# Kernel optimization log

Hardware: AMD Instinct MI355X
Metric: run time of the kernel (lower is better)

The kernel has to match this reference:

```python
import jax, jax.numpy as jnp
import numpy as np

N, L, A = 64, 196, 512      # batch, image regions, image feature dim
H, E, V = 512, 512, 30000   # lstm hidden, token embedding, vocab
T = 20                      # infer_seq_length
START = 1                   # _start token id


def setup_inputs() -> dict:
    key = jax.random.key(0)
    ks = jax.random.split(key, 16)
    s = lambda i, shape, scale=0.02: (jax.random.normal(ks[i], shape, jnp.float32) * scale)
    return {
        "batch_image_embbeding": jax.random.normal(ks[0], (N, L, A), jnp.float32),
        "emb_table": s(1, (V, E), 0.05),
        "Wh0": s(2, (A, H)), "bh0": jnp.zeros((H,), jnp.float32),
        "Wc0": s(3, (A, H)), "bc0": jnp.zeros((H,), jnp.float32),
        "Wa": s(4, (A, H)), "Ua": s(5, (H, H)), "ba": jnp.zeros((H,), jnp.float32),
        "va": s(6, (H,)),
        "Wb": s(7, (H, 1)), "bb": jnp.zeros((1,), jnp.float32),
        "Wx": s(8, (A + E, 4 * H)), "Wh": s(9, (H, 4 * H)),
        "b_lstm": jnp.zeros((4 * H,), jnp.float32),
        "Wout": s(10, (H, V)), "bout": jnp.zeros((V,), jnp.float32),
    }


def _decode(hl, emb_table, Wh0, bh0, Wc0, bc0, Wa, Ua, ba, va, Wb, bb,
            Wx, Wh, b_lstm, Wout, bout):
    mean_a = jnp.mean(hl, axis=1)                      # [N, A]
    h = jnp.tanh(mean_a @ Wh0 + bh0)                   # fc_init_h
    c = jnp.tanh(mean_a @ Wc0 + bc0)                   # fc_init_c
    tok = jnp.full((hl.shape[0],), START, jnp.int32)
    hl_Wa = jnp.einsum('nla,ah->nlh', hl, Wa)          # precompute attention keys

    def step(carry, _):
        h, c, tok = carry
        x_emb = emb_table[tok]                         # [N, E] embedding lookup
        # additive (Bahdanau) one-step attention
        e = jnp.einsum('nlh,h->nl', jnp.tanh(hl_Wa + (h @ Ua + ba)[:, None, :]), va)
        alpha = jax.nn.softmax(e, axis=-1)             # [N, L]
        z = jnp.einsum('nl,nla->na', alpha, hl)        # [N, A]
        z = z * jax.nn.sigmoid(h @ Wb + bb)            # beta gate
        x = jnp.concatenate([z, x_emb], axis=-1)       # [N, A+E]
        # single-step keras LSTM (gate order i, f, c, o)
        gates = x @ Wx + h @ Wh + b_lstm
        i, f, g, o = jnp.split(gates, 4, axis=-1)
        c = jax.nn.sigmoid(f) * c + jax.nn.sigmoid(i) * jnp.tanh(g)
        h = jax.nn.sigmoid(o) * jnp.tanh(c)
        logits = h @ Wout + bout                       # dropout is identity at inference
        tok = jnp.argmax(logits, axis=-1).astype(jnp.int32)
        return (h, c, tok), tok

    _, toks = jax.lax.scan(step, (h, c, tok), None, length=T)
    return jnp.transpose(toks, (1, 0))                 # [N, T]


def reference(batch_image_embbeding, emb_table, Wh0, bh0, Wc0, bc0, Wa, Ua, ba,
              va, Wb, bb, Wx, Wh, b_lstm, Wout, bout):
    return _decode(batch_image_embbeding, emb_table, Wh0, bh0, Wc0, bc0, Wa, Ua,
                   ba, va, Wb, bb, Wx, Wh, b_lstm, Wout, bout)
```

## Files before the change

kernel.cpp:

```cpp
#include <hip/hip_runtime.h>
#include <math.h>

#define NB   64
#define LL   196
#define AD   512
#define HD   512
#define VD   30000
#define TS   20
#define G4   2048
#define NBL  235
#define NC2  (NBL * 2)

typedef __bf16 bf16x8 __attribute__((ext_vector_type(8)));
typedef float  f32x4  __attribute__((ext_vector_type(4)));

__device__ __forceinline__ float fast_tanh(float x) {
    float e = __builtin_exp2f(x * 2.8853900817779268f);
    return 1.0f - 2.0f / (e + 1.0f);
}
__device__ __forceinline__ float fast_sigmoid(float x) {
    return 1.0f / (1.0f + __builtin_exp2f(-x * 1.4426950408889634f));
}
__device__ __forceinline__ float fast_exp(float x) {
    return __builtin_exp2f(x * 1.4426950408889634f);
}
__device__ __forceinline__ unsigned short f2bf(float f) {
    unsigned int u = __float_as_uint(f);
    u += 0x7fffu + ((u >> 16) & 1u);
    return (unsigned short)(u >> 16);
}
__device__ __forceinline__ void gload_lds16(const void* g, void* l) {
    __builtin_amdgcn_global_load_lds((const __attribute__((address_space(1))) void*)g,
                                     (__attribute__((address_space(3))) void*)l, 16, 0, 0);
}
__device__ __forceinline__ void top2_merge(float& v1, int& i1, float& v2, int& i2,
                                           float ov1, int oi1, float ov2, int oi2) {
    if (ov1 > v1 || (ov1 == v1 && oi1 < i1)) {
        float sv = v1; int si = i1;
        v1 = ov1; i1 = oi1;
        if (ov2 > sv || (ov2 == sv && oi2 < si)) { v2 = ov2; i2 = oi2; }
        else { v2 = sv; i2 = si; }
    } else {
        if (ov1 > v2 || (ov1 == v2 && oi1 < i2)) { v2 = ov1; i2 = oi1; }
    }
}

__global__ void k_init(const float* __restrict__ hl, const float* __restrict__ Wh0,
                       const float* __restrict__ bh0, const float* __restrict__ Wc0,
                       const float* __restrict__ bc0, float* __restrict__ h_ws,
                       float* __restrict__ c_ws, int* __restrict__ tok_ws) {
    __shared__ float mean_s[AD];
    int n = blockIdx.x, tid = threadIdx.x;
    for (int a = tid; a < AD; a += 256) {
        float acc = 0.f;
        const float* p = hl + ((size_t)n * LL) * AD + a;
        for (int l = 0; l < LL; ++l) acc += p[(size_t)l * AD];
        mean_s[a] = acc / 196.0f;
    }
    __syncthreads();
    for (int hh = tid; hh < HD; hh += 256) {
        float ah = bh0[hh], ac = bc0[hh];
        for (int k = 0; k < AD; ++k) {
            float m = mean_s[k];
            ah = fmaf(m, Wh0[k * HD + hh], ah);
            ac = fmaf(m, Wc0[k * HD + hh], ac);
        }
        h_ws[n * HD + hh] = fast_tanh(ah);
        c_ws[n * HD + hh] = fast_tanh(ac);
    }
    if (tid == 0) tok_ws[n] = 1;
}

__global__ void k_hlwa(const float* __restrict__ Amat, const float* __restrict__ Bmat,
                       float* __restrict__ Cmat) {
    __shared__ __attribute__((aligned(16))) float xt[64 * 64];
    __shared__ __attribute__((aligned(16))) float bs[64 * 68];
    int tid = threadIdx.x;
    int lane16 = tid & 15, rowg = tid >> 4;
    int m0 = blockIdx.x * 64, jb = blockIdx.y * 64;
    float acc[4][4] = {};
    for (int ch = 0; ch < 8; ++ch) {
        int kbase = ch * 64;
        __syncthreads();
        for (int it = 0; it < 4; ++it) {
            int k4 = tid & 15;
            int nrow = (tid >> 4) + it * 16;
            float4 v = *(const float4*)&Amat[(size_t)(m0 + nrow) * 512 + kbase + k4 * 4];
            int col = (nrow + k4 * 4) & 63;
            xt[(k4 * 4 + 0) * 64 + col] = v.x;
            xt[(k4 * 4 + 1) * 64 + col] = v.y;
            xt[(k4 * 4 + 2) * 64 + col] = v.z;
            xt[(k4 * 4 + 3) * 64 + col] = v.w;
        }
        for (int it = 0; it < 4; ++it) {
            int r = it * 16 + (tid >> 4);
            int c4 = (tid & 15) * 4;
            *(float4*)&bs[r * 68 + c4] = *(const float4*)&Bmat[(size_t)(kbase + r) * 512 + jb + c4];
        }
        __syncthreads();
#pragma unroll 8
        for (int kk = 0; kk < 64; ++kk) {
            float4 w4 = *(const float4*)&bs[kk * 68 + lane16 * 4];
            float4 h4 = *(const float4*)&xt[kk * 64 + ((rowg * 4 + (kk & ~3)) & 63)];
            float hv[4] = {h4.x, h4.y, h4.z, h4.w};
            float wv[4] = {w4.x, w4.y, w4.z, w4.w};
#pragma unroll
            for (int r = 0; r < 4; ++r)
#pragma unroll
                for (int j = 0; j < 4; ++j) acc[r][j] = fmaf(hv[r], wv[j], acc[r][j]);
        }
    }
    for (int r = 0; r < 4; ++r) {
        float4 o = {acc[r][0], acc[r][1], acc[r][2], acc[r][3]};
        *(float4*)&Cmat[(size_t)(m0 + rowg * 4 + r) * 512 + jb + lane16 * 4] = o;
    }
}

__global__ void k_wcvt(const float* __restrict__ Wout, unsigned short* __restrict__ WoutB) {
    int id = blockIdx.x * 256 + threadIdx.x;
    int lane = id & 63;
    int kb = (id >> 6) & 15;
    int vb = id >> 10;
    int v  = vb * 16 + (lane & 15);
    int k0 = kb * 32 + (lane >> 4) * 8;
    unsigned int pk[4];
#pragma unroll
    for (int p = 0; p < 4; ++p) {
        unsigned int lo = f2bf(Wout[(size_t)(k0 + 2 * p) * VD + v]);
        unsigned int hi = f2bf(Wout[(size_t)(k0 + 2 * p + 1) * VD + v]);
        pk[p] = lo | (hi << 16);
    }
    *(uint4*)&WoutB[(size_t)id * 8] = make_uint4(pk[0], pk[1], pk[2], pk[3]);
}

__global__ void k_hua(const float* __restrict__ h_ws, const float* __restrict__ Ua,
                      float* __restrict__ hua_part) {
    __shared__ __attribute__((aligned(16))) float xt[64 * 64];
    __shared__ __attribute__((aligned(16))) float us[64 * 68];
    int tid = threadIdx.x;
    int lane16 = tid & 15, rowg = tid >> 4;
    int s = blockIdx.x & 7, jt = blockIdx.x >> 3;
    int jb = jt * 64, kbase = s * 64;
    float acc[4][4] = {};
    for (int it = 0; it < 4; ++it) {
        int k4 = tid & 15;
        int nrow = (tid >> 4) + it * 16;
        float4 v = *(const float4*)&h_ws[nrow * 512 + kbase + k4 * 4];
        int col = (nrow + k4 * 4) & 63;
        xt[(k4 * 4 + 0) * 64 + col] = v.x;
        xt[(k4 * 4 + 1) * 64 + col] = v.y;
        xt[(k4 * 4 + 2) * 64 + col] = v.z;
        xt[(k4 * 4 + 3) * 64 + col] = v.w;
    }
    for (int it = 0; it < 4; ++it) {
        int r = it * 16 + (tid >> 4);
        int c4 = (tid & 15) * 4;
        *(float4*)&us[r * 68 + c4] = *(const float4*)&Ua[(size_t)(kbase + r) * 512 + jb + c4];
    }
    __syncthreads();
#pragma unroll 8
    for (int kk = 0; kk < 64; ++kk) {
        float4 w4 = *(const float4*)&us[kk * 68 + lane16 * 4];
        float4 h4 = *(const float4*)&xt[kk * 64 + ((rowg * 4 + (kk & ~3)) & 63)];
        float hv[4] = {h4.x, h4.y, h4.z, h4.w};
        float wv[4] = {w4.x, w4.y, w4.z, w4.w};
#pragma unroll
        for (int r = 0; r < 4; ++r)
#pragma unroll
            for (int j = 0; j < 4; ++j) acc[r][j] = fmaf(hv[r], wv[j], acc[r][j]);
    }
    float* gp = hua_part + (size_t)s * NB * HD;
    for (int r = 0; r < 4; ++r) {
        float4 o = {acc[r][0], acc[r][1], acc[r][2], acc[r][3]};
        *(float4*)&gp[(size_t)(rowg * 4 + r) * 512 + jb + lane16 * 4] = o;
    }
}

__global__ void k_att_e(const float* __restrict__ hlwa, const float* __restrict__ hua_part,
                        const float* __restrict__ ba, const float* __restrict__ va,
                        float* __restrict__ e_ws) {
    int n = blockIdx.x >> 2, q = blockIdx.x & 3;
    int tid = threadIdx.x;
    int wave = tid >> 6, lane = tid & 63;
    float4 ua_a = *(const float4*)&ba[lane * 4];
    float4 ua_b = *(const float4*)&ba[256 + lane * 4];
    for (int s = 0; s < 8; ++s) {
        const float* p = hua_part + (size_t)s * NB * HD + n * HD;
        float4 pa = *(const float4*)&p[lane * 4];
        float4 pb = *(const float4*)&p[256 + lane * 4];
        ua_a.x += pa.x; ua_a.y += pa.y; ua_a.z += pa.z; ua_a.w += pa.w;
        ua_b.x += pb.x; ua_b.y += pb.y; ua_b.z += pb.z; ua_b.w += pb.w;
    }
    float4 va_a = *(const float4*)&va[lane * 4];
    float4 va_b = *(const float4*)&va[256 + lane * 4];
    for (int ll = wave; ll < 49; ll += 4) {
        int l = q * 49 + ll;
        const float* base = hlwa + ((size_t)n * LL + l) * HD;
        float4 xa = *(const float4*)&base[lane * 4];
        float4 xb = *(const float4*)&base[256 + lane * 4];
        float s = 0.f;
        s = fmaf(fast_tanh(xa.x + ua_a.x), va_a.x, s);
        s = fmaf(fast_tanh(xa.y + ua_a.y), va_a.y, s);
        s = fmaf(fast_tanh(xa.z + ua_a.z), va_a.z, s);
        s = fmaf(fast_tanh(xa.w + ua_a.w), va_a.w, s);
        s = fmaf(fast_tanh(xb.x + ua_b.x), va_b.x, s);
        s = fmaf(fast_tanh(xb.y + ua_b.y), va_b.y, s);
        s = fmaf(fast_tanh(xb.z + ua_b.z), va_b.z, s);
        s = fmaf(fast_tanh(xb.w + ua_b.w), va_b.w, s);
        for (int m = 1; m < 64; m <<= 1) s += __shfl_xor(s, m, 64);
        if (lane == 0) e_ws[n * LL + l] = s;
    }
}

__global__ void k_soft_z(const float* __restrict__ e_ws, const float* __restrict__ hl,
                         const float* __restrict__ h_ws, const float* __restrict__ Wb,
                         const float* __restrict__ bb, float* __restrict__ z_ws) {
    __shared__ float red[256];
    __shared__ float alpha[256];
    __shared__ float zs[512];
    __shared__ float beta_s;
    int n = blockIdx.x, tid = threadIdx.x;
    float ev = (tid < LL) ? e_ws[n * LL + tid] : -INFINITY;
    red[tid] = ev;
    __syncthreads();
    for (int s = 128; s > 0; s >>= 1) {
        if (tid < s) red[tid] = fmaxf(red[tid], red[tid + s]);
        __syncthreads();
    }
    float m = red[0];
    __syncthreads();
    float a = (tid < LL) ? fast_exp(ev - m) : 0.f;
    red[tid] = a;
    __syncthreads();
    for (int s = 128; s > 0; s >>= 1) {
        if (tid < s) red[tid] += red[tid + s];
        __syncthreads();
    }
    float sum = red[0];
    alpha[tid] = a / sum;
    __syncthreads();
    float bp = h_ws[n * HD + tid] * Wb[tid] + h_ws[n * HD + 256 + tid] * Wb[256 + tid];
    red[tid] = bp;
    __syncthreads();
    for (int s = 128; s > 0; s >>= 1) {
        if (tid < s) red[tid] += red[tid + s];
        __syncthreads();
    }
    if (tid == 0) beta_s = fast_sigmoid(red[0] + bb[0]);
    int lq = tid >> 7, ai = tid & 127;
    const float* base = hl + ((size_t)n * LL) * AD + ai * 4;
    float4 acc4 = {0.f, 0.f, 0.f, 0.f};
    int l0 = lq * 98, l1 = l0 + 98;
    for (int l = l0; l < l1; ++l) {
        float al = alpha[l];
        float4 v = *(const float4*)&base[(size_t)l * AD];
        acc4.x = fmaf(al, v.x, acc4.x);
        acc4.y = fmaf(al, v.y, acc4.y);
        acc4.z = fmaf(al, v.z, acc4.z);
        acc4.w = fmaf(al, v.w, acc4.w);
    }
    if (lq == 1) *(float4*)&zs[ai * 4] = acc4;
    __syncthreads();
    if (lq == 0) {
        float4 o = *(const float4*)&zs[ai * 4];
        float b = beta_s;
        o.x = (o.x + acc4.x) * b;
        o.y = (o.y + acc4.y) * b;
        o.z = (o.z + acc4.z) * b;
        o.w = (o.w + acc4.w) * b;
        *(float4*)&z_ws[n * AD + ai * 4] = o;
    }
}

__global__ void k_gates(const float* __restrict__ z_ws, const float* __restrict__ emb,
                        const int* __restrict__ tok_ws, const float* __restrict__ h_ws,
                        const float* __restrict__ Wx, const float* __restrict__ Wh,
                        float* __restrict__ gates_part) {
    __shared__ __attribute__((aligned(16))) float xt[64 * 64];
    __shared__ __attribute__((aligned(16))) float wsl[64 * 68];
    int tid = threadIdx.x;
    int lane16 = tid & 15, rowg = tid >> 4;
    int s = blockIdx.x & 7, jt = blockIdx.x >> 3;
    int jb = jt * 64;
    float acc[4][4] = {};
    for (int ch = 0; ch < 3; ++ch) {
        int kbase = s * 192 + ch * 64;
        __syncthreads();
        for (int it = 0; it < 4; ++it) {
            int nrow = (tid >> 4) + it * 16;
            int k4 = tid & 15;
            int gk = kbase + k4 * 4;
            const float* src;
            if (gk < 512)       src = &z_ws[nrow * 512 + gk];
            else if (gk < 1024) src = &emb[(size_t)tok_ws[nrow] * 512 + (gk - 512)];
            else                src = &h_ws[nrow * 512 + (gk - 1024)];
            float4 v = *(const float4*)src;
            int col = (nrow + k4 * 4) & 63;
            xt[(k4 * 4 + 0) * 64 + col] = v.x;
            xt[(k4 * 4 + 1) * 64 + col] = v.y;
            xt[(k4 * 4 + 2) * 64 + col] = v.z;
            xt[(k4 * 4 + 3) * 64 + col] = v.w;
        }
        for (int it = 0; it < 4; ++it) {
            int r = it * 16 + (tid >> 4);
            int gk = kbase + r;
            const float* wrow = (gk < 1024) ? &Wx[(size_t)gk * G4] : &Wh[(size_t)(gk - 1024) * G4];
            int c4 = (tid & 15) * 4;
            *(float4*)&wsl[r * 68 + c4] = *(const float4*)&wrow[jb + c4];
        }
        __syncthreads();
#pragma unroll 8
        for (int kk = 0; kk < 64; ++kk) {
            float4 w4 = *(const float4*)&wsl[kk * 68 + lane16 * 4];
            float4 h4 = *(const float4*)&xt[kk * 64 + ((rowg * 4 + (kk & ~3)) & 63)];
            float hv[4] = {h4.x, h4.y, h4.z, h4.w};
            float wv[4] = {w4.x, w4.y, w4.z, w4.w};
#pragma unroll
            for (int r = 0; r < 4; ++r)
#pragma unroll
                for (int j = 0; j < 4; ++j) acc[r][j] = fmaf(hv[r], wv[j], acc[r][j]);
        }
    }
    float* gp = gates_part + (size_t)s * NB * G4;
    for (int r = 0; r < 4; ++r) {
        float4 o = {acc[r][0], acc[r][1], acc[r][2], acc[r][3]};
        *(float4*)&gp[(size_t)(rowg * 4 + r) * G4 + jb + lane16 * 4] = o;
    }
}

__global__ void k_lstm(const float* __restrict__ gates_part, const float* __restrict__ b_lstm,
                       float* __restrict__ h_ws, float* __restrict__ c_ws,
                       unsigned short* __restrict__ hB) {
    int idx = blockIdx.x * 256 + threadIdx.x;
    int n = idx >> 9, hh = idx & 511;
    float ig = b_lstm[hh], fg = b_lstm[512 + hh], gg = b_lstm[1024 + hh], og = b_lstm[1536 + hh];
    for (int s = 0; s < 8; ++s) {
        const float* gp = gates_part + (size_t)s * NB * G4 + (size_t)n * G4;
        ig += gp[hh]; fg += gp[512 + hh]; gg += gp[1024 + hh]; og += gp[1536 + hh];
    }
    float c = c_ws[idx];
    float cn = fast_sigmoid(fg) * c + fast_sigmoid(ig) * fast_tanh(gg);
    float hn = fast_sigmoid(og) * fast_tanh(cn);
    c_ws[idx] = cn;
    h_ws[idx] = hn;
    int mb = n >> 4, kb = hh >> 5;
    int lane = (n & 15) + ((hh >> 3) & 3) * 16;
    hB[(((size_t)mb * 16 + kb) * 64 + lane) * 8 + (hh & 7)] = f2bf(hn);
}

__global__ void k_logits(const unsigned short* __restrict__ hB,
                         const unsigned short* __restrict__ WoutB,
                         const float* __restrict__ bout,
                         float* __restrict__ pval, int* __restrict__ pidx) {
    __shared__ __attribute__((aligned(16))) unsigned short hs[4096 * 8];
    __shared__ float sv1[4][64]; __shared__ int si1[4][64];
    __shared__ float sv2[4][64]; __shared__ int si2[4][64];
    int tid = threadIdx.x;
    int w = tid >> 6, lane = tid & 63;
    int jb = blockIdx.x * 128;
    if (jb > VD - 128) jb = VD - 128;
#pragma unroll
    for (int i = 0; i < 16; ++i) {
        int base = i * 256 + w * 64;
        gload_lds16(&hB[(size_t)(base + lane) * 8], &hs[(size_t)base * 8]);
    }
    __syncthreads();
    int jbv = jb >> 4;
    int vbw = jbv + w * 2;
    const bf16x8* wP = (const bf16x8*)WoutB;
    const bf16x8* hP = (const bf16x8*)hs;
    f32x4 acc[2][4] = {};
#pragma unroll 2
    for (int kb = 0; kb < 16; ++kb) {
        bf16x8 b0 = wP[((size_t)vbw * 16 + kb) * 64 + lane];
        bf16x8 b1 = wP[((size_t)(vbw + 1) * 16 + kb) * 64 + lane];
        bf16x8 a0 = hP[(0 * 16 + kb) * 64 + lane];
        bf16x8 a1 = hP[(1 * 16 + kb) * 64 + lane];
        bf16x8 a2 = hP[(2 * 16 + kb) * 64 + lane];
        bf16x8 a3 = hP[(3 * 16 + kb) * 64 + lane];
        acc[0][0] = __builtin_amdgcn_mfma_f32_16x16x32_bf16(a0, b0, acc[0][0], 0, 0, 0);
        acc[0][1] = __builtin_amdgcn_mfma_f32_16x16x32_bf16(a1, b0, acc[0][1], 0, 0, 0);
        acc[0][2] = __builtin_amdgcn_mfma_f32_16x16x32_bf16(a2, b0, acc[0][2], 0, 0, 0);
        acc[0][3] = __builtin_amdgcn_mfma_f32_16x16x32_bf16(a3, b0, acc[0][3], 0, 0, 0);
        acc[1][0] = __builtin_amdgcn_mfma_f32_16x16x32_bf16(a0, b1, acc[1][0], 0, 0, 0);
        acc[1][1] = __builtin_amdgcn_mfma_f32_16x16x32_bf16(a1, b1, acc[1][1], 0, 0, 0);
        acc[1][2] = __builtin_amdgcn_mfma_f32_16x16x32_bf16(a2, b1, acc[1][2], 0, 0, 0);
        acc[1][3] = __builtin_amdgcn_mfma_f32_16x16x32_bf16(a3, b1, acc[1][3], 0, 0, 0);
    }
    float bo0 = bout[vbw * 16 + (lane & 15)];
    float bo1 = bout[(vbw + 1) * 16 + (lane & 15)];
    int colb = vbw * 16 + (lane & 15);
    int g = lane >> 4;
#pragma unroll
    for (int mbi = 0; mbi < 4; ++mbi) {
#pragma unroll
        for (int r = 0; r < 4; ++r) {
            int row = mbi * 16 + g * 4 + r;
            float v1 = acc[0][mbi][r] + bo0; int i1 = colb;
            float v2 = acc[1][mbi][r] + bo1; int i2 = colb + 16;
            if (v2 > v1 || (v2 == v1 && i2 < i1)) {
                float tv = v1; int ti = i1; v1 = v2; i1 = i2; v2 = tv; i2 = ti;
            }
            for (int m = 1; m < 16; m <<= 1) {
                float ov1 = __shfl_xor(v1, m, 64); int oi1 = __shfl_xor(i1, m, 64);
                float ov2 = __shfl_xor(v2, m, 64); int oi2 = __shfl_xor(i2, m, 64);
                top2_merge(v1, i1, v2, i2, ov1, oi1, ov2, oi2);
            }
            if ((lane & 15) == 0) {
                sv1[w][row] = v1; si1[w][row] = i1;
                sv2[w][row] = v2; si2[w][row] = i2;
            }
        }
    }
    __syncthreads();
    if (tid < 64) {
        float v1 = sv1[0][tid]; int i1 = si1[0][tid];
        float v2 = sv2[0][tid]; int i2 = si2[0][tid];
        for (int q = 1; q < 4; ++q)
            top2_merge(v1, i1, v2, i2, sv1[q][tid], si1[q][tid], sv2[q][tid], si2[q][tid]);
        pval[(size_t)tid * NC2 + blockIdx.x * 2 + 0] = v1;
        pval[(size_t)tid * NC2 + blockIdx.x * 2 + 1] = v2;
        pidx[(size_t)tid * NC2 + blockIdx.x * 2 + 0] = i1;
        pidx[(size_t)tid * NC2 + blockIdx.x * 2 + 1] = i2;
    }
}

__global__ void k_argmax(const float* __restrict__ pval, const int* __restrict__ pidx,
                         const float* __restrict__ h_ws, const float* __restrict__ Wout,
                         const float* __restrict__ bout, int* __restrict__ tok_ws,
                         int* __restrict__ out, int t) {
    int n = blockIdx.x, lane = threadIdx.x;
    const float* pv = pval + (size_t)n * NC2;
    const int*   pi = pidx + (size_t)n * NC2;
    float cv[8]; int ci[8];
#pragma unroll
    for (int q = 0; q < 8; ++q) {
        int i = q * 64 + lane;
        bool ok = i < NC2;
        cv[q] = ok ? pv[i] : -INFINITY;
        ci[q] = ok ? pi[i] : 0x7fffffff;
    }
    int picks[4];
#pragma unroll
    for (int c = 0; c < 4; ++c) {
        float best = -INFINITY; int bi = 0x7fffffff;
#pragma unroll
        for (int q = 0; q < 8; ++q) {
            bool skip = false;
#pragma unroll
            for (int p = 0; p < 4; ++p) skip = skip || (p < c && ci[q] == picks[p]);
            if (!skip && (cv[q] > best || (cv[q] == best && ci[q] < bi))) { best = cv[q]; bi = ci[q]; }
        }
        for (int m = 1; m < 64; m <<= 1) {
            float ov = __shfl_xor(best, m, 64);
            int   oi = __shfl_xor(bi, m, 64);
            if (ov > best || (ov == best && oi < bi)) { best = ov; bi = oi; }
        }
        picks[c] = bi;
    }
    const float* hr = h_ws + (size_t)n * HD;
    float hv[8];
#pragma unroll
    for (int j = 0; j < 8; ++j) hv[j] = hr[lane * 8 + j];
    float s0 = 0.f, s1 = 0.f, s2 = 0.f, s3 = 0.f;
#pragma unroll
    for (int j = 0; j < 8; ++j) {
        size_t krow = (size_t)(lane * 8 + j) * VD;
        s0 = fmaf(hv[j], Wout[krow + picks[0]], s0);
        s1 = fmaf(hv[j], Wout[krow + picks[1]], s1);
        s2 = fmaf(hv[j], Wout[krow + picks[2]], s2);
        s3 = fmaf(hv[j], Wout[krow + picks[3]], s3);
    }
    for (int m = 1; m < 64; m <<= 1) {
        s0 += __shfl_xor(s0, m, 64);
        s1 += __shfl_xor(s1, m, 64);
        s2 += __shfl_xor(s2, m, 64);
        s3 += __shfl_xor(s3, m, 64);
    }
    if (lane == 0) {
        float pex[4] = {s0 + bout[picks[0]], s1 + bout[picks[1]],
                        s2 + bout[picks[2]], s3 + bout[picks[3]]};
        float best = pex[0]; int bi = picks[0];
        for (int c = 1; c < 4; ++c)
            if (pex[c] > best || (pex[c] == best && picks[c] < bi)) { best = pex[c]; bi = picks[c]; }
        tok_ws[n] = bi;
        out[n * TS + t] = bi;
    }
}

extern "C" void kernel_launch(void* const* d_in, const int* in_sizes, int n_in,
                              void* d_out, int out_size, void* d_ws, size_t ws_size,
                              hipStream_t stream) {
    const float* hl     = (const float*)d_in[0];
    const float* emb    = (const float*)d_in[1];
    const float* Wh0    = (const float*)d_in[2];
    const float* bh0    = (const float*)d_in[3];
    const float* Wc0    = (const float*)d_in[4];
    const float* bc0    = (const float*)d_in[5];
    const float* Wa     = (const float*)d_in[6];
    const float* Ua     = (const float*)d_in[7];
    const float* ba     = (const float*)d_in[8];
    const float* va     = (const float*)d_in[9];
    const float* Wb     = (const float*)d_in[10];
    const float* bb     = (const float*)d_in[11];
    const float* Wx     = (const float*)d_in[12];
    const float* Wh     = (const float*)d_in[13];
    const float* b_lstm = (const float*)d_in[14];
    const float* Wout   = (const float*)d_in[15];
    const float* bout   = (const float*)d_in[16];

    float* ws         = (float*)d_ws;
    float* hlwa       = ws;
    float* h_ws       = ws + 6422528;
    float* c_ws       = h_ws + 32768;
    float* z_ws       = c_ws + 32768;
    float* e_ws       = z_ws + 32768;
    int*   tok_ws     = (int*)(e_ws + 12544);
    float* hua_part   = e_ws + 12544 + 64;
    float* gates_part = hua_part + 262144;
    float* pval       = gates_part + 1048576;
    int*   pidx       = (int*)(pval + 64 * NC2);
    unsigned short* hB    = (unsigned short*)(pval + 2 * 64 * NC2);
    unsigned short* WoutB = (unsigned short*)(pval + 2 * 64 * NC2 + 16384);
    int*   out        = (int*)d_out;

    k_init<<<64, 256, 0, stream>>>(hl, Wh0, bh0, Wc0, bc0, h_ws, c_ws, tok_ws);
    k_wcvt<<<7500, 256, 0, stream>>>(Wout, WoutB);
    k_hlwa<<<dim3(196, 8), 256, 0, stream>>>(hl, Wa, hlwa);
    for (int t = 0; t < TS; ++t) {
        k_hua<<<64, 256, 0, stream>>>(h_ws, Ua, hua_part);
        k_att_e<<<256, 256, 0, stream>>>(hlwa, hua_part, ba, va, e_ws);
        k_soft_z<<<64, 256, 0, stream>>>(e_ws, hl, h_ws, Wb, bb, z_ws);
        k_gates<<<256, 256, 0, stream>>>(z_ws, emb, tok_ws, h_ws, Wx, Wh, gates_part);
        k_lstm<<<128, 256, 0, stream>>>(gates_part, b_lstm, h_ws, c_ws, hB);
        k_logits<<<NBL, 256, 0, stream>>>(hB, WoutB, bout, pval, pidx);
        k_argmax<<<64, 64, 0, stream>>>(pval, pidx, h_ws, Wout, bout, tok_ws, out, t);
    }
}
```

Baseline: 2.087 ms.

## Fuse decode loop into persistent kernel with grid barriers and overlapped attention

Replaces the 140 per-step kernel launches with one persistent 256-block kernel that uses atomic-counter grid barriers between phases. The next step's attention-key projection and energy computation run on idle blocks while other blocks compute logits and argmax, which shortens the serial chain. The logits stage now stages h in two LDS halves so it fits the shared buffer. It also rebalances the attention energy work over 3 quarters. The risks are that it depends on all 256 blocks being co-resident and that each barrier spins on the atomic counter.

```diff
diff --git a/kernel.cpp b/kernel.cpp
--- a/kernel.cpp
+++ b/kernel.cpp
@@ -10,6 +10,7 @@
 #define G4   2048
 #define NBL  235
 #define NC2  (NBL * 2)
+#define NBLK 256
 
 typedef __bf16 bf16x8 __attribute__((ext_vector_type(8)));
 typedef float  f32x4  __attribute__((ext_vector_type(4)));
@@ -45,12 +46,26 @@
     }
 }
 
+__device__ __forceinline__ void gridbar(unsigned* cnt, unsigned target) {
+    __syncthreads();
+    if (threadIdx.x == 0) {
+        __threadfence();
+        __hip_atomic_fetch_add(cnt, 1u, __ATOMIC_ACQ_REL, __HIP_MEMORY_SCOPE_AGENT);
+        while (__hip_atomic_load(cnt, __ATOMIC_ACQUIRE, __HIP_MEMORY_SCOPE_AGENT) < target) {
+            __builtin_amdgcn_s_sleep(2);
+        }
+    }
+    __syncthreads();
+}
+
 __global__ void k_init(const float* __restrict__ hl, const float* __restrict__ Wh0,
                        const float* __restrict__ bh0, const float* __restrict__ Wc0,
                        const float* __restrict__ bc0, float* __restrict__ h_ws,
-                       float* __restrict__ c_ws, int* __restrict__ tok_ws) {
+                       float* __restrict__ c_ws, int* __restrict__ tok_ws,
+                       unsigned* __restrict__ barcnt) {
     __shared__ float mean_s[AD];
     int n = blockIdx.x, tid = threadIdx.x;
+    if (n == 0 && tid == 0) *barcnt = 0u;
     for (int a = tid; a < AD; a += 256) {
         float acc = 0.f;
         const float* p = hl + ((size_t)n * LL) * AD + a;
@@ -133,13 +148,14 @@
     *(uint4*)&WoutB[(size_t)id * 8] = make_uint4(pk[0], pk[1], pk[2], pk[3]);
 }
 
-__global__ void k_hua(const float* __restrict__ h_ws, const float* __restrict__ Ua,
-                      float* __restrict__ hua_part) {
-    __shared__ __attribute__((aligned(16))) float xt[64 * 64];
-    __shared__ __attribute__((aligned(16))) float us[64 * 68];
-    int tid = threadIdx.x;
+
+__device__ __forceinline__ void do_hua(int b, int tid, float* smem,
+        const float* __restrict__ h_ws, const float* __restrict__ Ua,
+        float* __restrict__ hua_part) {
+    float* xt = smem;
+    float* us = smem + 4096;
     int lane16 = tid & 15, rowg = tid >> 4;
-    int s = blockIdx.x & 7, jt = blockIdx.x >> 3;
+    int s = b & 7, jt = b >> 3;
     int jb = jt * 64, kbase = s * 64;
     float acc[4][4] = {};
     for (int it = 0; it < 4; ++it) {
@@ -176,11 +192,11 @@
     }
 }
 
-__global__ void k_att_e(const float* __restrict__ hlwa, const float* __restrict__ hua_part,
-                        const float* __restrict__ ba, const float* __restrict__ va,
-                        float* __restrict__ e_ws) {
-    int n = blockIdx.x >> 2, q = blockIdx.x & 3;
-    int tid = threadIdx.x;
+__device__ __forceinline__ void do_att_e(int b, int tid,
+        const float* __restrict__ hlwa, const float* __restrict__ hua_part,
+        const float* __restrict__ ba, const float* __restrict__ va,
+        float* __restrict__ e_ws) {
+    int n = b & 63, q = b >> 6;
     int wave = tid >> 6, lane = tid & 63;
     float4 ua_a = *(const float4*)&ba[lane * 4];
     float4 ua_b = *(const float4*)&ba[256 + lane * 4];
@@ -193,8 +209,8 @@
     }
     float4 va_a = *(const float4*)&va[lane * 4];
     float4 va_b = *(const float4*)&va[256 + lane * 4];
-    for (int ll = wave; ll < 49; ll += 4) {
-        int l = q * 49 + ll;
+    int lstart = q * 66, lend = (q == 2) ? LL : (q * 66 + 66);
+    for (int l = lstart + wave; l < lend; l += 4) {
         const float* base = hlwa + ((size_t)n * LL + l) * HD;
         float4 xa = *(const float4*)&base[lane * 4];
         float4 xb = *(const float4*)&base[256 + lane * 4];
@@ -212,14 +228,13 @@
     }
 }
 
-__global__ void k_soft_z(const float* __restrict__ e_ws, const float* __restrict__ hl,
-                         const float* __restrict__ h_ws, const float* __restrict__ Wb,
-                         const float* __restrict__ bb, float* __restrict__ z_ws) {
-    __shared__ float red[256];
-    __shared__ float alpha[256];
-    __shared__ float zs[512];
-    __shared__ float beta_s;
-    int n = blockIdx.x, tid = threadIdx.x;
+__device__ __forceinline__ void do_soft_z(int n, int tid, float* smem,
+        const float* __restrict__ e_ws, const float* __restrict__ hl,
+        const float* __restrict__ h_ws, const float* __restrict__ Wb,
+        const float* __restrict__ bb, float* __restrict__ z_ws) {
+    float* red = smem;
+    float* alpha = smem + 256;
+    float* zs = smem + 512;
     float ev = (tid < LL) ? e_ws[n * LL + tid] : -INFINITY;
     red[tid] = ev;
     __syncthreads();
@@ -246,7 +261,7 @@
         if (tid < s) red[tid] += red[tid + s];
         __syncthreads();
     }
-    if (tid == 0) beta_s = fast_sigmoid(red[0] + bb[0]);
+    if (tid == 0) smem[1024] = fast_sigmoid(red[0] + bb[0]);
     int lq = tid >> 7, ai = tid & 127;
     const float* base = hl + ((size_t)n * LL) * AD + ai * 4;
     float4 acc4 = {0.f, 0.f, 0.f, 0.f};
@@ -263,7 +278,7 @@
     __syncthreads();
     if (lq == 0) {
         float4 o = *(const float4*)&zs[ai * 4];
-        float b = beta_s;
+        float b = smem[1024];
         o.x = (o.x + acc4.x) * b;
         o.y = (o.y + acc4.y) * b;
         o.z = (o.z + acc4.z) * b;
@@ -272,15 +287,15 @@
     }
 }
 
-__global__ void k_gates(const float* __restrict__ z_ws, const float* __restrict__ emb,
-                        const int* __restrict__ tok_ws, const float* __restrict__ h_ws,
-                        const float* __restrict__ Wx, const float* __restrict__ Wh,
-                        float* __restrict__ gates_part) {
-    __shared__ __attribute__((aligned(16))) float xt[64 * 64];
-    __shared__ __attribute__((aligned(16))) float wsl[64 * 68];
-    int tid = threadIdx.x;
+__device__ __forceinline__ void do_gates(int b, int tid, float* smem,
+        const float* __restrict__ z_ws, const float* __restrict__ emb,
+        const int* __restrict__ tok_ws, const float* __restrict__ h_ws,
+        const float* __restrict__ Wx, const float* __restrict__ Wh,
+        float* __restrict__ gates_part) {
+    float* xt = smem;
+    float* wsl = smem + 4096;
     int lane16 = tid & 15, rowg = tid >> 4;
-    int s = blockIdx.x & 7, jt = blockIdx.x >> 3;
+    int s = b & 7, jt = b >> 3;
     int jb = jt * 64;
     float acc[4][4] = {};
     for (int ch = 0; ch < 3; ++ch) {
@@ -328,10 +343,11 @@
     }
 }
 
-__global__ void k_lstm(const float* __restrict__ gates_part, const float* __restrict__ b_lstm,
-                       float* __restrict__ h_ws, float* __restrict__ c_ws,
-                       unsigned short* __restrict__ hB) {
-    int idx = blockIdx.x * 256 + threadIdx.x;
+__device__ __forceinline__ void do_lstm(int b, int tid,
+        const float* __restrict__ gates_part, const float* __restrict__ b_lstm,
+        float* __restrict__ h_ws, float* __restrict__ c_ws,
+        unsigned short* __restrict__ hB) {
+    int idx = b * 256 + tid;
     int n = idx >> 9, hh = idx & 511;
     float ig = b_lstm[hh], fg = b_lstm[512 + hh], gg = b_lstm[1024 + hh], og = b_lstm[1536 + hh];
     for (int s = 0; s < 8; ++s) {
@@ -348,44 +364,47 @@
     hB[(((size_t)mb * 16 + kb) * 64 + lane) * 8 + (hh & 7)] = f2bf(hn);
 }
 
-__global__ void k_logits(const unsigned short* __restrict__ hB,
-                         const unsigned short* __restrict__ WoutB,
-                         const float* __restrict__ bout,
-                         float* __restrict__ pval, int* __restrict__ pidx) {
-    __shared__ __attribute__((aligned(16))) unsigned short hs[4096 * 8];
-    __shared__ float sv1[4][64]; __shared__ int si1[4][64];
-    __shared__ float sv2[4][64]; __shared__ int si2[4][64];
-    int tid = threadIdx.x;
+__device__ __forceinline__ void do_logits(int tile, int tid, float* smem,
+        const unsigned short* __restrict__ hB, const unsigned short* __restrict__ WoutB,
+        const float* __restrict__ bout, float* __restrict__ pval, int* __restrict__ pidx) {
+    unsigned short* hs = (unsigned short*)smem;
+    float* sv1 = smem + 8192; float* sv2 = smem + 8448;
+    int* si1 = (int*)(smem + 8704); int* si2 = (int*)(smem + 8960);
     int w = tid >> 6, lane = tid & 63;
-    int jb = blockIdx.x * 128;
+    int jb = tile * 128;
     if (jb > VD - 128) jb = VD - 128;
-#pragma unroll
-    for (int i = 0; i < 16; ++i) {
-        int base = i * 256 + w * 64;
-        gload_lds16(&hB[(size_t)(base + lane) * 8], &hs[(size_t)base * 8]);
-    }
-    __syncthreads();
-    int jbv = jb >> 4;
-    int vbw = jbv + w * 2;
+    int vbw = (jb >> 4) + w * 2;
     const bf16x8* wP = (const bf16x8*)WoutB;
     const bf16x8* hP = (const bf16x8*)hs;
     f32x4 acc[2][4] = {};
+    for (int hf = 0; hf < 2; ++hf) {
+        __syncthreads();
+#pragma unroll
+        for (int i = 0; i < 8; ++i) {
+            int sbase = i * 256 + w * 64;
+            int mb = sbase >> 9, kb2 = (sbase >> 6) & 7;
+            int gslot = (mb * 16 + hf * 8 + kb2) * 64;
+            gload_lds16(&hB[(size_t)(gslot + lane) * 8], &hs[(size_t)sbase * 8]);
+        }
+        __syncthreads();
 #pragma unroll 2
-    for (int kb = 0; kb < 16; ++kb) {
-        bf16x8 b0 = wP[((size_t)vbw * 16 + kb) * 64 + lane];
-        bf16x8 b1 = wP[((size_t)(vbw + 1) * 16 + kb) * 64 + lane];
-        bf16x8 a0 = hP[(0 * 16 + kb) * 64 + lane];
-        bf16x8 a1 = hP[(1 * 16 + kb) * 64 + lane];
-        bf16x8 a2 = hP[(2 * 16 + kb) * 64 + lane];
-        bf16x8 a3 = hP[(3 * 16 + kb) * 64 + lane];
-        acc[0][0] = __builtin_amdgcn_mfma_f32_16x16x32_bf16(a0, b0, acc[0][0], 0, 0, 0);
-        acc[0][1] = __builtin_amdgcn_mfma_f32_16x16x32_bf16(a1, b0, acc[0][1], 0, 0, 0);
-        acc[0][2] = __builtin_amdgcn_mfma_f32_16x16x32_bf16(a2, b0, acc[0][2], 0, 0, 0);
-        acc[0][3] = __builtin_amdgcn_mfma_f32_16x16x32_bf16(a3, b0, acc[0][3], 0, 0, 0);
-        acc[1][0] = __builtin_amdgcn_mfma_f32_16x16x32_bf16(a0, b1, acc[1][0], 0, 0, 0);
-        acc[1][1] = __builtin_amdgcn_mfma_f32_16x16x32_bf16(a1, b1, acc[1][1], 0, 0, 0);
-        acc[1][2] = __builtin_amdgcn_mfma_f32_16x16x32_bf16(a2, b1, acc[1][2], 0, 0, 0);
-        acc[1][3] = __builtin_amdgcn_mfma_f32_16x16x32_bf16(a3, b1, acc[1][3], 0, 0, 0);
+        for (int kb2 = 0; kb2 < 8; ++kb2) {
+            int kb = hf * 8 + kb2;
+            bf16x8 b0 = wP[((size_t)vbw * 16 + kb) * 64 + lane];
+            bf16x8 b1 = wP[((size_t)(vbw + 1) * 16 + kb) * 64 + lane];
+            bf16x8 a0 = hP[(0 * 8 + kb2) * 64 + lane];
+            bf16x8 a1 = hP[(1 * 8 + kb2) * 64 + lane];
+            bf16x8 a2 = hP[(2 * 8 + kb2) * 64 + lane];
+            bf16x8 a3 = hP[(3 * 8 + kb2) * 64 + lane];
+            acc[0][0] = __builtin_amdgcn_mfma_f32_16x16x32_bf16(a0, b0, acc[0][0], 0, 0, 0);
+            acc[0][1] = __builtin_amdgcn_mfma_f32_16x16x32_bf16(a1, b0, acc[0][1], 0, 0, 0);
+            acc[0][2] = __builtin_amdgcn_mfma_f32_16x16x32_bf16(a2, b0, acc[0][2], 0, 0, 0);
+            acc[0][3] = __builtin_amdgcn_mfma_f32_16x16x32_bf16(a3, b0, acc[0][3], 0, 0, 0);
+            acc[1][0] = __builtin_amdgcn_mfma_f32_16x16x32_bf16(a0, b1, acc[1][0], 0, 0, 0);
+            acc[1][1] = __builtin_amdgcn_mfma_f32_16x16x32_bf16(a1, b1, acc[1][1], 0, 0, 0);
+            acc[1][2] = __builtin_amdgcn_mfma_f32_16x16x32_bf16(a2, b1, acc[1][2], 0, 0, 0);
+            acc[1][3] = __builtin_amdgcn_mfma_f32_16x16x32_bf16(a3, b1, acc[1][3], 0, 0, 0);
+        }
     }
     float bo0 = bout[vbw * 16 + (lane & 15)];
     float bo1 = bout[(vbw + 1) * 16 + (lane & 15)];
@@ -407,29 +426,31 @@
                 top2_merge(v1, i1, v2, i2, ov1, oi1, ov2, oi2);
             }
             if ((lane & 15) == 0) {
-                sv1[w][row] = v1; si1[w][row] = i1;
-                sv2[w][row] = v2; si2[w][row] = i2;
+                sv1[w * 64 + row] = v1; si1[w * 64 + row] = i1;
+                sv2[w * 64 + row] = v2; si2[w * 64 + row] = i2;
             }
         }
     }
     __syncthreads();
     if (tid < 64) {
-        float v1 = sv1[0][tid]; int i1 = si1[0][tid];
-        float v2 = sv2[0][tid]; int i2 = si2[0][tid];
+        float v1 = sv1[tid]; int i1 = si1[tid];
+        float v2 = sv2[tid]; int i2 = si2[tid];
         for (int q = 1; q < 4; ++q)
-            top2_merge(v1, i1, v2, i2, sv1[q][tid], si1[q][tid], sv2[q][tid], si2[q][tid]);
-        pval[(size_t)tid * NC2 + blockIdx.x * 2 + 0] = v1;
-        pval[(size_t)tid * NC2 + blockIdx.x * 2 + 1] = v2;
-        pidx[(size_t)tid * NC2 + blockIdx.x * 2 + 0] = i1;
-        pidx[(size_t)tid * NC2 + blockIdx.x * 2 + 1] = i2;
-    }
-}
-
-__global__ void k_argmax(const float* __restrict__ pval, const int* __restrict__ pidx,
-                         const float* __restrict__ h_ws, const float* __restrict__ Wout,
-                         const float* __restrict__ bout, int* __restrict__ tok_ws,
-                         int* __restrict__ out, int t) {
-    int n = blockIdx.x, lane = threadIdx.x;
+            top2_merge(v1, i1, v2, i2, sv1[q * 64 + tid], si1[q * 64 + tid],
+                       sv2[q * 64 + tid], si2[q * 64 + tid]);
+        pval[(size_t)tid * NC2 + tile * 2 + 0] = v1;
+        pval[(size_t)tid * NC2 + tile * 2 + 1] = v2;
+        pidx[(size_t)tid * NC2 + tile * 2 + 0] = i1;
+        pidx[(size_t)tid * NC2 + tile * 2 + 1] = i2;
+    }
+}
+
+__device__ __forceinline__ void do_argmax(int n, int tid, int t,
+        const float* __restrict__ pval, const int* __restrict__ pidx,
+        const float* __restrict__ h_ws, const float* __restrict__ Wout,
+        const float* __restrict__ bout, int* __restrict__ tok_ws, int* __restrict__ out) {
+    if (tid >= 64) return;
+    int lane = tid;
     const float* pv = pval + (size_t)n * NC2;
     const int*   pi = pidx + (size_t)n * NC2;
     float cv[8]; int ci[8];
@@ -486,6 +507,48 @@
         tok_ws[n] = bi;
         out[n * TS + t] = bi;
     }
+}
+
+__global__ void __launch_bounds__(256)
+k_steps(const float* hl, const float* emb, const float* Ua, const float* ba,
+        const float* va, const float* Wb, const float* bb, const float* Wx,
+        const float* Wh, const float* b_lstm, const float* Wout, const float* bout,
+        const unsigned short* WoutB, const float* hlwa,
+        float* h_ws, float* c_ws, float* z_ws, float* e_ws, int* tok_ws,
+        float* hua_part, float* gates_part, float* pval, int* pidx,
+        unsigned short* hB, int* out, unsigned* barcnt) {
+    __shared__ __attribute__((aligned(16))) float smem[9472];
+    int blk = blockIdx.x, tid = threadIdx.x;
+    unsigned bar_target = 0;
+#define GSYNC() do { bar_target += NBLK; gridbar(barcnt, bar_target); } while (0)
+
+    if (blk < 64) do_hua(blk, tid, smem, h_ws, Ua, hua_part);
+    GSYNC();
+    if (blk < 192) do_att_e(blk, tid, hlwa, hua_part, ba, va, e_ws);
+    GSYNC();
+    if (blk < 64) do_soft_z(blk, tid, smem, e_ws, hl, h_ws, Wb, bb, z_ws);
+    GSYNC();
+
+    for (int t = 0; t < TS; ++t) {
+        do_gates(blk, tid, smem, z_ws, emb, tok_ws, h_ws, Wx, Wh, gates_part);
+        GSYNC();
+        if (blk < 128) do_lstm(blk, tid, gates_part, b_lstm, h_ws, c_ws, hB);
+        GSYNC();
+        if (blk < 192) {
+            do_logits(blk, tid, smem, hB, WoutB, bout, pval, pidx);
+            if (blk < NBL - 192) do_logits(blk + 192, tid, smem, hB, WoutB, bout, pval, pidx);
+        } else if (t < TS - 1) {
+            do_hua(blk - 192, tid, smem, h_ws, Ua, hua_part);
+        }
+        GSYNC();
+        if (blk < 64) do_argmax(blk, tid, t, pval, pidx, h_ws, Wout, bout, tok_ws, out);
+        else if (t < TS - 1) do_att_e(blk - 64, tid, hlwa, hua_part, ba, va, e_ws);
+        GSYNC();
+        if (blk < 64 && t < TS - 1)
+            do_soft_z(blk, tid, smem, e_ws, hl, h_ws, Wb, bb, z_ws);
+        GSYNC();
+    }
+#undef GSYNC
 }
 
 extern "C" void kernel_launch(void* const* d_in, const int* in_sizes, int n_in,
@@ -522,18 +585,14 @@
     int*   pidx       = (int*)(pval + 64 * NC2);
     unsigned short* hB    = (unsigned short*)(pval + 2 * 64 * NC2);
     unsigned short* WoutB = (unsigned short*)(pval + 2 * 64 * NC2 + 16384);
+    unsigned* barcnt  = (unsigned*)(ws + 15600704);
     int*   out        = (int*)d_out;
 
-    k_init<<<64, 256, 0, stream>>>(hl, Wh0, bh0, Wc0, bc0, h_ws, c_ws, tok_ws);
+    k_init<<<64, 256, 0, stream>>>(hl, Wh0, bh0, Wc0, bc0, h_ws, c_ws, tok_ws, barcnt);
     k_wcvt<<<7500, 256, 0, stream>>>(Wout, WoutB);
     k_hlwa<<<dim3(196, 8), 256, 0, stream>>>(hl, Wa, hlwa);
-    for (int t = 0; t < TS; ++t) {
-        k_hua<<<64, 256, 0, stream>>>(h_ws, Ua, hua_part);
-        k_att_e<<<256, 256, 0, stream>>>(hlwa, hua_part, ba, va, e_ws);
-        k_soft_z<<<64, 256, 0, stream>>>(e_ws, hl, h_ws, Wb, bb, z_ws);
-        k_gates<<<256, 256, 0, stream>>>(z_ws, emb, tok_ws, h_ws, Wx, Wh, gates_part);
-        k_lstm<<<128, 256, 0, stream>>>(gates_part, b_lstm, h_ws, c_ws, hB);
-        k_logits<<<NBL, 256, 0, stream>>>(hB, WoutB, bout, pval, pidx);
-        k_argmax<<<64, 64, 0, stream>>>(pval, pidx, h_ws, Wout, bout, tok_ws, out, t);
-    }
-}
+    k_steps<<<NBLK, 256, 0, stream>>>(hl, emb, Ua, ba, va, Wb, bb, Wx, Wh, b_lstm,
+                                      Wout, bout, WoutB, hlwa, h_ws, c_ws, z_ws, e_ws,
+                                      tok_ws, hua_part, gates_part, pval, pidx, hB, out,
+                                      barcnt);
+}
```

Result: slower. 8.281 ms (+296.7%).

## Merge attention-query projection and scores into logits/argmax launches to cut launches

Applied to the files above, without the earlier changes.

The per-step attention work for the next step (h@Ua and the score computation) only depends on the new h. It is now run as extra blocks inside the logits kernel and the argmax kernel, and the first step's attention is peeled before the loop. This removes two kernel launches per step and lets the independent work share the GPU with the logits GEMM. The cost is a larger LDS allocation in the merged logits kernel, which may lower occupancy, and argmax blocks now launch 256 threads, of which 192 exit at once.

```diff
diff --git a/kernel.cpp b/kernel.cpp
--- a/kernel.cpp
+++ b/kernel.cpp
@@ -176,11 +176,11 @@
     }
 }
 
-__global__ void k_att_e(const float* __restrict__ hlwa, const float* __restrict__ hua_part,
-                        const float* __restrict__ ba, const float* __restrict__ va,
-                        float* __restrict__ e_ws) {
-    int n = blockIdx.x >> 2, q = blockIdx.x & 3;
-    int tid = threadIdx.x;
+__device__ __forceinline__ void atte_body(int b, int tid,
+        const float* __restrict__ hlwa, const float* __restrict__ hua_part,
+        const float* __restrict__ ba, const float* __restrict__ va,
+        float* __restrict__ e_ws) {
+    int n = b >> 2, q = b & 3;
     int wave = tid >> 6, lane = tid & 63;
     float4 ua_a = *(const float4*)&ba[lane * 4];
     float4 ua_b = *(const float4*)&ba[256 + lane * 4];
@@ -212,6 +212,12 @@
     }
 }
 
+__global__ void k_att_e(const float* __restrict__ hlwa, const float* __restrict__ hua_part,
+                        const float* __restrict__ ba, const float* __restrict__ va,
+                        float* __restrict__ e_ws) {
+    atte_body(blockIdx.x, threadIdx.x, hlwa, hua_part, ba, va, e_ws);
+}
+
 __global__ void k_soft_z(const float* __restrict__ e_ws, const float* __restrict__ hl,
                          const float* __restrict__ h_ws, const float* __restrict__ Wb,
                          const float* __restrict__ bb, float* __restrict__ z_ws) {
@@ -348,88 +354,144 @@
     hB[(((size_t)mb * 16 + kb) * 64 + lane) * 8 + (hh & 7)] = f2bf(hn);
 }
 
-__global__ void k_logits(const unsigned short* __restrict__ hB,
+__global__ void k_loghua(const unsigned short* __restrict__ hB,
                          const unsigned short* __restrict__ WoutB,
                          const float* __restrict__ bout,
-                         float* __restrict__ pval, int* __restrict__ pidx) {
-    __shared__ __attribute__((aligned(16))) unsigned short hs[4096 * 8];
-    __shared__ float sv1[4][64]; __shared__ int si1[4][64];
-    __shared__ float sv2[4][64]; __shared__ int si2[4][64];
-    int tid = threadIdx.x;
-    int w = tid >> 6, lane = tid & 63;
-    int jb = blockIdx.x * 128;
-    if (jb > VD - 128) jb = VD - 128;
-#pragma unroll
-    for (int i = 0; i < 16; ++i) {
-        int base = i * 256 + w * 64;
-        gload_lds16(&hB[(size_t)(base + lane) * 8], &hs[(size_t)base * 8]);
-    }
-    __syncthreads();
-    int jbv = jb >> 4;
-    int vbw = jbv + w * 2;
-    const bf16x8* wP = (const bf16x8*)WoutB;
-    const bf16x8* hP = (const bf16x8*)hs;
-    f32x4 acc[2][4] = {};
+                         float* __restrict__ pval, int* __restrict__ pidx,
+                         const float* __restrict__ h_ws, const float* __restrict__ Ua,
+                         float* __restrict__ hua_part) {
+    __shared__ __attribute__((aligned(16))) char smem[69632];
+    int blk = blockIdx.x, tid = threadIdx.x;
+    if (blk < NBL) {
+        unsigned short* hs = (unsigned short*)smem;
+        float* sv1 = (float*)(smem + 65536);
+        float* sv2 = (float*)(smem + 66560);
+        int*   si1 = (int*)(smem + 67584);
+        int*   si2 = (int*)(smem + 68608);
+        int w = tid >> 6, lane = tid & 63;
+        int jb = blk * 128;
+        if (jb > VD - 128) jb = VD - 128;
+#pragma unroll
+        for (int i = 0; i < 16; ++i) {
+            int base = i * 256 + w * 64;
+            gload_lds16(&hB[(size_t)(base + lane) * 8], &hs[(size_t)base * 8]);
+        }
+        __syncthreads();
+        int vbw = (jb >> 4) + w * 2;
+        const bf16x8* wP = (const bf16x8*)WoutB;
+        const bf16x8* hP = (const bf16x8*)hs;
+        f32x4 acc[2][4] = {};
 #pragma unroll 2
-    for (int kb = 0; kb < 16; ++kb) {
-        bf16x8 b0 = wP[((size_t)vbw * 16 + kb) * 64 + lane];
-        bf16x8 b1 = wP[((size_t)(vbw + 1) * 16 + kb) * 64 + lane];
-        bf16x8 a0 = hP[(0 * 16 + kb) * 64 + lane];
-        bf16x8 a1 = hP[(1 * 16 + kb) * 64 + lane];
-        bf16x8 a2 = hP[(2 * 16 + kb) * 64 + lane];
-        bf16x8 a3 = hP[(3 * 16 + kb) * 64 + lane];
-        acc[0][0] = __builtin_amdgcn_mfma_f32_16x16x32_bf16(a0, b0, acc[0][0], 0, 0, 0);
-        acc[0][1] = __builtin_amdgcn_mfma_f32_16x16x32_bf16(a1, b0, acc[0][1], 0, 0, 0);
-        acc[0][2] = __builtin_amdgcn_mfma_f32_16x16x32_bf16(a2, b0, acc[0][2], 0, 0, 0);
-        acc[0][3] = __builtin_amdgcn_mfma_f32_16x16x32_bf16(a3, b0, acc[0][3], 0, 0, 0);
-        acc[1][0] = __builtin_amdgcn_mfma_f32_16x16x32_bf16(a0, b1, acc[1][0], 0, 0, 0);
-        acc[1][1] = __builtin_amdgcn_mfma_f32_16x16x32_bf16(a1, b1, acc[1][1], 0, 0, 0);
-        acc[1][2] = __builtin_amdgcn_mfma_f32_16x16x32_bf16(a2, b1, acc[1][2], 0, 0, 0);
-        acc[1][3] = __builtin_amdgcn_mfma_f32_16x16x32_bf16(a3, b1, acc[1][3], 0, 0, 0);
-    }
-    float bo0 = bout[vbw * 16 + (lane & 15)];
-    float bo1 = bout[(vbw + 1) * 16 + (lane & 15)];
-    int colb = vbw * 16 + (lane & 15);
-    int g = lane >> 4;
-#pragma unroll
-    for (int mbi = 0; mbi < 4; ++mbi) {
-#pragma unroll
+        for (int kb = 0; kb < 16; ++kb) {
+            bf16x8 b0 = wP[((size_t)vbw * 16 + kb) * 64 + lane];
+            bf16x8 b1 = wP[((size_t)(vbw + 1) * 16 + kb) * 64 + lane];
+            bf16x8 a0 = hP[(0 * 16 + kb) * 64 + lane];
+            bf16x8 a1 = hP[(1 * 16 + kb) * 64 + lane];
+            bf16x8 a2 = hP[(2 * 16 + kb) * 64 + lane];
+            bf16x8 a3 = hP[(3 * 16 + kb) * 64 + lane];
+            acc[0][0] = __builtin_amdgcn_mfma_f32_16x16x32_bf16(a0, b0, acc[0][0], 0, 0, 0);
+            acc[0][1] = __builtin_amdgcn_mfma_f32_16x16x32_bf16(a1, b0, acc[0][1], 0, 0, 0);
+            acc[0][2] = __builtin_amdgcn_mfma_f32_16x16x32_bf16(a2, b0, acc[0][2], 0, 0, 0);
+            acc[0][3] = __builtin_amdgcn_mfma_f32_16x16x32_bf16(a3, b0, acc[0][3], 0, 0, 0);
+            acc[1][0] = __builtin_amdgcn_mfma_f32_16x16x32_bf16(a0, b1, acc[1][0], 0, 0, 0);
+            acc[1][1] = __builtin_amdgcn_mfma_f32_16x16x32_bf16(a1, b1, acc[1][1], 0, 0, 0);
+            acc[1][2] = __builtin_amdgcn_mfma_f32_16x16x32_bf16(a2, b1, acc[1][2], 0, 0, 0);
+            acc[1][3] = __builtin_amdgcn_mfma_f32_16x16x32_bf16(a3, b1, acc[1][3], 0, 0, 0);
+        }
+        float bo0 = bout[vbw * 16 + (lane & 15)];
+        float bo1 = bout[(vbw + 1) * 16 + (lane & 15)];
+        int colb = vbw * 16 + (lane & 15);
+        int g = lane >> 4;
+#pragma unroll
+        for (int mbi = 0; mbi < 4; ++mbi) {
+#pragma unroll
+            for (int r = 0; r < 4; ++r) {
+                int row = mbi * 16 + g * 4 + r;
+                float v1 = acc[0][mbi][r] + bo0; int i1 = colb;
+                float v2 = acc[1][mbi][r] + bo1; int i2 = colb + 16;
+                if (v2 > v1 || (v2 == v1 && i2 < i1)) {
+                    float tv = v1; int ti = i1; v1 = v2; i1 = i2; v2 = tv; i2 = ti;
+                }
+                for (int m = 1; m < 16; m <<= 1) {
+                    float ov1 = __shfl_xor(v1, m, 64); int oi1 = __shfl_xor(i1, m, 64);
+                    float ov2 = __shfl_xor(v2, m, 64); int oi2 = __shfl_xor(i2, m, 64);
+                    top2_merge(v1, i1, v2, i2, ov1, oi1, ov2, oi2);
+                }
+                if ((lane & 15) == 0) {
+                    sv1[w * 64 + row] = v1; si1[w * 64 + row] = i1;
+                    sv2[w * 64 + row] = v2; si2[w * 64 + row] = i2;
+                }
+            }
+        }
+        __syncthreads();
+        if (tid < 64) {
+            float v1 = sv1[tid]; int i1 = si1[tid];
+            float v2 = sv2[tid]; int i2 = si2[tid];
+            for (int q = 1; q < 4; ++q)
+                top2_merge(v1, i1, v2, i2, sv1[q * 64 + tid], si1[q * 64 + tid],
+                           sv2[q * 64 + tid], si2[q * 64 + tid]);
+            pval[(size_t)tid * NC2 + blk * 2 + 0] = v1;
+            pval[(size_t)tid * NC2 + blk * 2 + 1] = v2;
+            pidx[(size_t)tid * NC2 + blk * 2 + 0] = i1;
+            pidx[(size_t)tid * NC2 + blk * 2 + 1] = i2;
+        }
+    } else {
+        float* xt = (float*)smem;
+        float* us = (float*)(smem + 16384);
+        int b = blk - NBL;
+        int lane16 = tid & 15, rowg = tid >> 4;
+        int s = b & 7, jt = b >> 3;
+        int jb = jt * 64, kbase = s * 64;
+        float acc[4][4] = {};
+        for (int it = 0; it < 4; ++it) {
+            int k4 = tid & 15;
+            int nrow = (tid >> 4) + it * 16;
+            float4 v = *(const float4*)&h_ws[nrow * 512 + kbase + k4 * 4];
+            int col = (nrow + k4 * 4) & 63;
+            xt[(k4 * 4 + 0) * 64 + col] = v.x;
+            xt[(k4 * 4 + 1) * 64 + col] = v.y;
+            xt[(k4 * 4 + 2) * 64 + col] = v.z;
+            xt[(k4 * 4 + 3) * 64 + col] = v.w;
+        }
+        for (int it = 0; it < 4; ++it) {
+            int r = it * 16 + (tid >> 4);
+            int c4 = (tid & 15) * 4;
+            *(float4*)&us[r * 68 + c4] = *(const float4*)&Ua[(size_t)(kbase + r) * 512 + jb + c4];
+        }
+        __syncthreads();
+#pragma unroll 8
+        for (int kk = 0; kk < 64; ++kk) {
+            float4 w4 = *(const float4*)&us[kk * 68 + lane16 * 4];
+            float4 h4 = *(const float4*)&xt[kk * 64 + ((rowg * 4 + (kk & ~3)) & 63)];
+            float hv[4] = {h4.x, h4.y, h4.z, h4.w};
+            float wv[4] = {w4.x, w4.y, w4.z, w4.w};
+#pragma unroll
+            for (int r = 0; r < 4; ++r)
+#pragma unroll
+                for (int j = 0; j < 4; ++j) acc[r][j] = fmaf(hv[r], wv[j], acc[r][j]);
+        }
+        float* gp = hua_part + (size_t)s * NB * HD;
         for (int r = 0; r < 4; ++r) {
-            int row = mbi * 16 + g * 4 + r;
-            float v1 = acc[0][mbi][r] + bo0; int i1 = colb;
-            float v2 = acc[1][mbi][r] + bo1; int i2 = colb + 16;
-            if (v2 > v1 || (v2 == v1 && i2 < i1)) {
-                float tv = v1; int ti = i1; v1 = v2; i1 = i2; v2 = tv; i2 = ti;
-            }
-            for (int m = 1; m < 16; m <<= 1) {
-                float ov1 = __shfl_xor(v1, m, 64); int oi1 = __shfl_xor(i1, m, 64);
-                float ov2 = __shfl_xor(v2, m, 64); int oi2 = __shfl_xor(i2, m, 64);
-                top2_merge(v1, i1, v2, i2, ov1, oi1, ov2, oi2);
-            }
-            if ((lane & 15) == 0) {
-                sv1[w][row] = v1; si1[w][row] = i1;
-                sv2[w][row] = v2; si2[w][row] = i2;
-            }
-        }
-    }
-    __syncthreads();
-    if (tid < 64) {
-        float v1 = sv1[0][tid]; int i1 = si1[0][tid];
-        float v2 = sv2[0][tid]; int i2 = si2[0][tid];
-        for (int q = 1; q < 4; ++q)
-            top2_merge(v1, i1, v2, i2, sv1[q][tid], si1[q][tid], sv2[q][tid], si2[q][tid]);
-        pval[(size_t)tid * NC2 + blockIdx.x * 2 + 0] = v1;
-        pval[(size_t)tid * NC2 + blockIdx.x * 2 + 1] = v2;
-        pidx[(size_t)tid * NC2 + blockIdx.x * 2 + 0] = i1;
-        pidx[(size_t)tid * NC2 + blockIdx.x * 2 + 1] = i2;
-    }
-}
-
-__global__ void k_argmax(const float* __restrict__ pval, const int* __restrict__ pidx,
+            float4 o = {acc[r][0], acc[r][1], acc[r][2], acc[r][3]};
+            *(float4*)&gp[(size_t)(rowg * 4 + r) * 512 + jb + lane16 * 4] = o;
+        }
+    }
+}
+
+__global__ void k_axatte(const float* __restrict__ pval, const int* __restrict__ pidx,
                          const float* __restrict__ h_ws, const float* __restrict__ Wout,
                          const float* __restrict__ bout, int* __restrict__ tok_ws,
-                         int* __restrict__ out, int t) {
-    int n = blockIdx.x, lane = threadIdx.x;
+                         int* __restrict__ out, int t,
+                         const float* __restrict__ hlwa, const float* __restrict__ hua_part,
+                         const float* __restrict__ ba, const float* __restrict__ va,
+                         float* __restrict__ e_ws) {
+    int blk = blockIdx.x, tid = threadIdx.x;
+    if (blk >= 64) {
+        atte_body(blk - 64, tid, hlwa, hua_part, ba, va, e_ws);
+        return;
+    }
+    if (tid >= 64) return;
+    int n = blk, lane = tid;
     const float* pv = pval + (size_t)n * NC2;
     const int*   pi = pidx + (size_t)n * NC2;
     float cv[8]; int ci[8];
@@ -527,13 +589,18 @@
     k_init<<<64, 256, 0, stream>>>(hl, Wh0, bh0, Wc0, bc0, h_ws, c_ws, tok_ws);
     k_wcvt<<<7500, 256, 0, stream>>>(Wout, WoutB);
     k_hlwa<<<dim3(196, 8), 256, 0, stream>>>(hl, Wa, hlwa);
+    k_hua<<<64, 256, 0, stream>>>(h_ws, Ua, hua_part);
+    k_att_e<<<256, 256, 0, stream>>>(hlwa, hua_part, ba, va, e_ws);
+    k_soft_z<<<64, 256, 0, stream>>>(e_ws, hl, h_ws, Wb, bb, z_ws);
     for (int t = 0; t < TS; ++t) {
-        k_hua<<<64, 256, 0, stream>>>(h_ws, Ua, hua_part);
-        k_att_e<<<256, 256, 0, stream>>>(hlwa, hua_part, ba, va, e_ws);
-        k_soft_z<<<64, 256, 0, stream>>>(e_ws, hl, h_ws, Wb, bb, z_ws);
         k_gates<<<256, 256, 0, stream>>>(z_ws, emb, tok_ws, h_ws, Wx, Wh, gates_part);
         k_lstm<<<128, 256, 0, stream>>>(gates_part, b_lstm, h_ws, c_ws, hB);
-        k_logits<<<NBL, 256, 0, stream>>>(hB, WoutB, bout, pval, pidx);
-        k_argmax<<<64, 64, 0, stream>>>(pval, pidx, h_ws, Wout, bout, tok_ws, out, t);
-    }
-}
+        k_loghua<<<NBL + 64, 256, 0, stream>>>(hB, WoutB, bout, pval, pidx,
+                                               h_ws, Ua, hua_part);
+        k_axatte<<<(t == TS - 1) ? 64 : 320, 256, 0, stream>>>(
+            pval, pidx, h_ws, Wout, bout, tok_ws, out, t,
+            hlwa, hua_part, ba, va, e_ws);
+        if (t < TS - 1)
+            k_soft_z<<<64, 256, 0, stream>>>(e_ws, hl, h_ws, Wb, bb, z_ws);
+    }
+}
```

Result: faster. 1.766 ms (-15.4%).
